# Optimization experiments

Hardware: AMD Instinct MI355X
Metric: run time of the kernel (lower is better)

## Reference

```python
import jax, jax.numpy as jnp
import numpy as np

N_NODES = 20000
N_GRAPH = 256
NODE_DIM = 128
MULS = (128, 64, 32)       # node irreps: 128x0e + 64x1o + 32x2e
HC = 32                    # hidden channels per irrep
HIDDEN_DIM = 64
N_PATH = 9                 # feasible uuw paths into 0e+1e+2e
W_NUMEL = N_PATH * HC * HC # 9216


def _tables():
    # real Clebsch-Gordan tensors built from cartesian tensor algebra,
    # normalized so that sum(C**2) = 2*l_out + 1 (component normalization)
    eps = np.zeros((3, 3, 3))
    eps[0, 1, 2] = eps[1, 2, 0] = eps[2, 0, 1] = 1.0
    eps[0, 2, 1] = eps[2, 1, 0] = eps[1, 0, 2] = -1.0
    s2, s6 = 1 / np.sqrt(2), 1 / np.sqrt(6)
    Q2 = np.zeros((5, 3, 3))  # orthonormal basis of traceless symmetric 3x3
    Q2[0, 0, 1] = Q2[0, 1, 0] = s2          # xy
    Q2[1, 1, 2] = Q2[1, 2, 1] = s2          # yz
    Q2[2, 0, 0] = Q2[2, 1, 1] = -s6; Q2[2, 2, 2] = 2 * s6  # z2
    Q2[3, 0, 2] = Q2[3, 2, 0] = s2          # xz
    Q2[4, 0, 0] = s2; Q2[4, 1, 1] = -s2     # x2-y2

    def nrm(C, l3):
        return C * np.sqrt((2 * l3 + 1) / (C ** 2).sum())

    C000 = np.ones((1, 1, 1))
    C022 = np.eye(5)[None, :, :]
    C110 = np.eye(3).reshape(3, 3, 1) / np.sqrt(3)
    C111 = eps / np.sqrt(2)
    C112 = np.transpose(Q2, (1, 2, 0))
    C202 = np.eye(5)[:, None, :]
    C220 = np.eye(5).reshape(5, 5, 1) / np.sqrt(5)
    M = np.einsum('iab,jdb->ijad', Q2, Q2)  # [5,5,3,3]
    C221 = nrm(np.einsum('cad,ijad->ijc', eps, M), 1)
    S = 0.5 * (M + np.transpose(M, (0, 1, 3, 2)))
    S = S - np.trace(S, axis1=2, axis2=3)[..., None, None] * np.eye(3) / 3.0
    C222 = nrm(np.einsum('kad,ijad->ijk', Q2, S), 2)
    # sph2cart change of basis: 9 spherical comps (0e+1e+2e) -> 3x3 cartesian
    Qc = np.zeros((3, 3, 9))
    Qc[:, :, 0] = np.eye(3) / np.sqrt(3)        # isotropic part
    Qc[:, :, 1:4] = eps / np.sqrt(2)            # antisymmetric part
    Qc[:, :, 4:9] = np.transpose(Q2, (1, 2, 0)) # symmetric traceless part
    return [C000, C022, C110, C111, C112, C202, C220, C221, C222], Qc

_CGS, _QC = _tables()


def setup_inputs() -> dict:
    key = jax.random.key(0)
    ks = jax.random.split(key, 12)
    f32 = jnp.float32
    d_sph = MULS[0] + 3 * MULS[1] + 5 * MULS[2]  # 480
    return {
        'x_scalar': jax.random.normal(ks[0], (N_NODES, NODE_DIM), f32),
        'x_spherical': jax.random.normal(ks[1], (N_NODES, d_sph), f32),
        'batch': jnp.sort(jax.random.randint(ks[2], (N_NODES,), 0, N_GRAPH)),
        'W0e': jax.random.normal(ks[3], (MULS[0], HC), f32),
        'W1o': jax.random.normal(ks[4], (MULS[1], HC), f32),
        'W2e': jax.random.normal(ks[5], (MULS[2], HC), f32),
        'Wm1': jax.random.normal(ks[6], (NODE_DIM, HIDDEN_DIM), f32) / np.sqrt(NODE_DIM),
        'bm1': jnp.zeros((HIDDEN_DIM,), f32),
        'Wm2': jax.random.normal(ks[7], (HIDDEN_DIM, W_NUMEL), f32) / np.sqrt(HIDDEN_DIM),
        'bm2': jnp.zeros((W_NUMEL,), f32),
        'P0': jax.random.normal(ks[8], (3 * HC,), f32),
        'P1': jax.random.normal(ks[9], (2 * HC,), f32),
        'P2': jax.random.normal(ks[10], (4 * HC,), f32),
    }


def reference(x_scalar, x_spherical, batch, W0e, W1o, W2e, Wm1, bm1, Wm2, bm2, P0, P1, P2):
    n = x_scalar.shape[0]
    m0, m1, m2 = MULS
    # split node features into irrep blocks
    x0 = x_spherical[:, :m0, None]                        # [N,128,1] 0e
    x1 = x_spherical[:, m0:m0 + 3 * m1].reshape(n, m1, 3) # [N,64,3]  1o
    x2 = x_spherical[:, m0 + 3 * m1:].reshape(n, m2, 5)   # [N,32,5]  2e
    # pre_lin: per-irrep channel mixing (e3nn-style 1/sqrt(fan_in))
    h = [jnp.einsum('num,uv->nvm', x, W) / np.sqrt(W.shape[0])
         for x, W in ((x0, W0e), (x1, W1o), (x2, W2e))]   # each [N,32,2l+1]
    # per-node tensor-product weights from scalar features
    w = (jax.nn.silu(x_scalar @ Wm1 + bm1) @ Wm2 + bm2).reshape(n, N_PATH, HC, HC)
    # uuw tensor product, path order matches _CGS
    paths = ((0, 0), (0, 2), (1, 1), (1, 1), (1, 1), (2, 0), (2, 2), (2, 2), (2, 2))
    inv_u = 1.0 / np.sqrt(HC)
    outs = []
    for k, (i, j) in enumerate(paths):
        C = jnp.asarray(_CGS[k], x_scalar.dtype)
        outs.append(jnp.einsum('pqr,nup,nuq,nuw->nwr', C, h[i], h[j], w[:, k]) * inv_u)
    # post_lin: combine paths of each output l into a single channel
    y0 = jnp.einsum('num,u->nm', jnp.concatenate([outs[0], outs[2], outs[6]], 1), P0) / np.sqrt(3 * HC)
    y1 = jnp.einsum('num,u->nm', jnp.concatenate([outs[3], outs[7]], 1), P1) / np.sqrt(2 * HC)
    y2 = jnp.einsum('num,u->nm', jnp.concatenate([outs[1], outs[4], outs[5], outs[8]], 1), P2) / np.sqrt(4 * HC)
    sph = jnp.concatenate([y0, y1, y2], axis=1)           # [N,9]
    cart = jnp.einsum('abi,ni->nab', jnp.asarray(_QC, sph.dtype), sph)  # [N,3,3]
    red = jax.ops.segment_sum(cart, batch, num_segments=N_GRAPH)        # [B,3,3]
    # if_trace is False (if_iso=False): roll every non-batch dim by 1
    return jnp.roll(jnp.roll(red, 1, axis=1), 1, axis=2)
```

## Files before the change

kernel.cpp:

```cpp
#include <hip/hip_runtime.h>
#include <math.h>

#define OFF_W2P 0
#define OFF_B2P 12288
#define WS_FLOATS 12480

#define SC_Y0 0.0180421959121758f
#define SC_Y2 0.015625f
#define S2f 0.70710678118654752f
#define S6f 0.40824829046386302f
#define TWOS2f 1.41421356237309505f
#define TWOS6f 0.81649658092772603f
#define ISQRT3 0.57735026918962576f
#define ISQRT5 0.44721359549995794f
#define H0SC 0.08838834764831845f
#define H1SC 0.125f
#define H2SC 0.17677669529663689f

#define COMP(v, q) ((q) == 0 ? (v).x : (q) == 1 ? (v).y : (q) == 2 ? (v).z : (v).w)

__device__ static inline float dot32(const float* __restrict__ a,
                                     const float* __restrict__ b) {
  const float4* a4 = (const float4*)a;
  const float4* b4 = (const float4*)b;
  float acc = 0.f;
#pragma unroll
  for (int q = 0; q < 8; ++q) {
    float4 x = a4[q], y = b4[q];
    acc += x.x * y.x + x.y * y.y + x.z * y.z + x.w * y.w;
  }
  return acc;
}

__global__ __launch_bounds__(256) void prep_kernel(
    const float* __restrict__ Wm2, const float* __restrict__ bm2,
    const float* __restrict__ P0, const float* __restrict__ P2,
    float* __restrict__ ws, float* __restrict__ out) {
  int j = blockIdx.x * 256 + threadIdx.x;
  if (j < 2304) out[j] = 0.f;

  if (j < 12288) {
    const int c = j / 192, o = j % 192;
    const int s = o >> 5, u = o & 31;
    int k; const float* P; float sc;
    switch (s) {
      case 0: k = 0; P = P0;      sc = SC_Y0; break;
      case 1: k = 1; P = P2;      sc = SC_Y2; break;
      case 2: k = 2; P = P0 + 32; sc = SC_Y0; break;
      case 3: k = 4; P = P2 + 32; sc = SC_Y2; break;
      case 4: k = 6; P = P0 + 64; sc = SC_Y0; break;
      default: k = 8; P = P2 + 96; sc = SC_Y2; break;
    }
    float acc = dot32(Wm2 + c * 9216 + k * 1024 + u * 32, P);
    if (s == 1) acc += dot32(Wm2 + c * 9216 + 5 * 1024 + u * 32, P2 + 64);
    ws[OFF_W2P + j] = acc * sc;
  } else if (j < 12480) {
    const int o = j - 12288;
    const int s = o >> 5, u = o & 31;
    int k; const float* P; float sc;
    switch (s) {
      case 0: k = 0; P = P0;      sc = SC_Y0; break;
      case 1: k = 1; P = P2;      sc = SC_Y2; break;
      case 2: k = 2; P = P0 + 32; sc = SC_Y0; break;
      case 3: k = 4; P = P2 + 32; sc = SC_Y2; break;
      case 4: k = 6; P = P0 + 64; sc = SC_Y0; break;
      default: k = 8; P = P2 + 96; sc = SC_Y2; break;
    }
    float acc = dot32(bm2 + k * 1024 + u * 32, P);
    if (s == 1) acc += dot32(bm2 + 5 * 1024 + u * 32, P2 + 64);
    ws[OFF_B2P + o] = acc * sc;
  }
}

__global__ __launch_bounds__(256, 3) void fused_kernel(
    const float* __restrict__ xs_g, const float* __restrict__ xsph,
    const float* __restrict__ W0e, const float* __restrict__ W1o,
    const float* __restrict__ W2e,
    const float* __restrict__ Wm1, const float* __restrict__ bm1,
    const float* __restrict__ ws, const int* __restrict__ batch,
    float* __restrict__ out, const float norm2) {
  __shared__ __align__(16) float smem[11952];
  float (*xp)[484] = (float (*)[484])smem;
  float (*hi2)[64] = (float (*)[64])(smem + 7744);
  float (*Vt)[193] = (float (*)[193])(smem + 8768);
  float (*sphs)[6] = (float (*)[6])(smem + 11856);

  const int tid = threadIdx.x;
  const int n0 = blockIdx.x * 16;

  float4 st[7];
  float4 st7;
#pragma unroll
  for (int k = 0; k < 7; ++k) {
    const int d = tid + k * 256;
    const int r = d / 120, c = d % 120;
    st[k] = *(const float4*)(xsph + (size_t)(n0 + r) * 480 + c * 4);
  }
  if (tid < 128) {
    const int d = tid + 1792;
    const int r = d / 120, c = d % 120;
    st7 = *(const float4*)(xsph + (size_t)(n0 + r) * 480 + c * 4);
  }

  {
    const int n = tid >> 4, c0 = (tid & 15) * 4;
    const float* xr = xs_g + (size_t)(n0 + n) * 128;
    float a0 = 0.f, a1 = 0.f, a2 = 0.f, a3 = 0.f;
#pragma unroll 4
    for (int mq = 0; mq < 32; ++mq) {
      const float4 xv = *(const float4*)(xr + mq * 4);
      const float4 w0 = *(const float4*)(Wm1 + (mq * 4 + 0) * 64 + c0);
      const float4 w1 = *(const float4*)(Wm1 + (mq * 4 + 1) * 64 + c0);
      const float4 w2 = *(const float4*)(Wm1 + (mq * 4 + 2) * 64 + c0);
      const float4 w3 = *(const float4*)(Wm1 + (mq * 4 + 3) * 64 + c0);
      a0 += xv.x * w0.x + xv.y * w1.x + xv.z * w2.x + xv.w * w3.x;
      a1 += xv.x * w0.y + xv.y * w1.y + xv.z * w2.y + xv.w * w3.y;
      a2 += xv.x * w0.z + xv.y * w1.z + xv.z * w2.z + xv.w * w3.z;
      a3 += xv.x * w0.w + xv.y * w1.w + xv.z * w2.w + xv.w * w3.w;
    }
    const float4 bb = *(const float4*)(bm1 + c0);
    const float z0 = a0 + bb.x, z1 = a1 + bb.y, z2 = a2 + bb.z, z3 = a3 + bb.w;
    float4 s;
    s.x = z0 / (1.f + __expf(-z0));
    s.y = z1 / (1.f + __expf(-z1));
    s.z = z2 / (1.f + __expf(-z2));
    s.w = z3 / (1.f + __expf(-z3));
    *(float4*)&hi2[n][c0] = s;
  }

#pragma unroll
  for (int k = 0; k < 7; ++k) {
    const int d = tid + k * 256;
    const int r = d / 120, c = d % 120;
    *(float4*)&xp[r][c * 4] = st[k];
  }
  if (tid < 128) {
    const int d = tid + 1792;
    const int r = d / 120, c = d % 120;
    *(float4*)&xp[r][c * 4] = st7;
  }
  __syncthreads();

  const int n = tid >> 3, ug = tid & 7, u0 = ug * 4;
  float4 acc0 = {0.f, 0.f, 0.f, 0.f};
  float4 acc1[3];
  float4 acc2[5];

  if (tid < 128) {
    const float* row = xp[n];
#pragma unroll 4
    for (int mq = 0; mq < 32; ++mq) {
      const float4 xv = *(const float4*)(row + mq * 4);
#pragma unroll
      for (int r = 0; r < 4; ++r) {
        const float4 w = *(const float4*)(W0e + (mq * 4 + r) * 32 + u0);
        const float xr = COMP(xv, r);
        acc0.x += xr * w.x; acc0.y += xr * w.y;
        acc0.z += xr * w.z; acc0.w += xr * w.w;
      }
    }
#pragma unroll
    for (int j = 0; j < 3; ++j) acc1[j] = make_float4(0.f, 0.f, 0.f, 0.f);
#pragma unroll 2
    for (int mq = 0; mq < 16; ++mq) {
      const float4 b0 = *(const float4*)(row + 128 + mq * 12);
      const float4 b1 = *(const float4*)(row + 128 + mq * 12 + 4);
      const float4 b2 = *(const float4*)(row + 128 + mq * 12 + 8);
      const float xa[12] = {b0.x, b0.y, b0.z, b0.w, b1.x, b1.y, b1.z, b1.w,
                            b2.x, b2.y, b2.z, b2.w};
#pragma unroll
      for (int mm = 0; mm < 4; ++mm) {
        const float4 w = *(const float4*)(W1o + (mq * 4 + mm) * 32 + u0);
#pragma unroll
        for (int j = 0; j < 3; ++j) {
          const float xr = xa[mm * 3 + j];
          acc1[j].x += xr * w.x; acc1[j].y += xr * w.y;
          acc1[j].z += xr * w.z; acc1[j].w += xr * w.w;
        }
      }
    }
#pragma unroll
    for (int j = 0; j < 5; ++j) acc2[j] = make_float4(0.f, 0.f, 0.f, 0.f);
#pragma unroll 2
    for (int mq = 0; mq < 8; ++mq) {
      const float4 c0v = *(const float4*)(row + 320 + mq * 20);
      const float4 c1v = *(const float4*)(row + 320 + mq * 20 + 4);
      const float4 c2v = *(const float4*)(row + 320 + mq * 20 + 8);
      const float4 c3v = *(const float4*)(row + 320 + mq * 20 + 12);
      const float4 c4v = *(const float4*)(row + 320 + mq * 20 + 16);
      const float xa[20] = {c0v.x, c0v.y, c0v.z, c0v.w, c1v.x, c1v.y, c1v.z, c1v.w,
                            c2v.x, c2v.y, c2v.z, c2v.w, c3v.x, c3v.y, c3v.z, c3v.w,
                            c4v.x, c4v.y, c4v.z, c4v.w};
#pragma unroll
      for (int mm = 0; mm < 4; ++mm) {
        const float4 w = *(const float4*)(W2e + (mq * 4 + mm) * 32 + u0);
#pragma unroll
        for (int j = 0; j < 5; ++j) {
          const float xr = xa[mm * 5 + j];
          acc2[j].x += xr * w.x; acc2[j].y += xr * w.y;
          acc2[j].z += xr * w.z; acc2[j].w += xr * w.w;
        }
      }
    }
  } else {
    const int j = tid - 128;
    const bool two = (j < 64);
    const int o2 = j + 128;
    float accA[16], accB[16];
    {
      const float bA = ws[OFF_B2P + j];
#pragma unroll
      for (int nn = 0; nn < 16; ++nn) accA[nn] = bA;
    }
    if (two) {
      const float bB = ws[OFF_B2P + o2];
#pragma unroll
      for (int nn = 0; nn < 16; ++nn) accB[nn] = bB;
    }
    for (int c4 = 0; c4 < 64; c4 += 4) {
      const float wA0 = ws[OFF_W2P + (c4 + 0) * 192 + j];
      const float wA1 = ws[OFF_W2P + (c4 + 1) * 192 + j];
      const float wA2 = ws[OFF_W2P + (c4 + 2) * 192 + j];
      const float wA3 = ws[OFF_W2P + (c4 + 3) * 192 + j];
      float wB0, wB1, wB2, wB3;
      if (two) {
        wB0 = ws[OFF_W2P + (c4 + 0) * 192 + o2];
        wB1 = ws[OFF_W2P + (c4 + 1) * 192 + o2];
        wB2 = ws[OFF_W2P + (c4 + 2) * 192 + o2];
        wB3 = ws[OFF_W2P + (c4 + 3) * 192 + o2];
      }
#pragma unroll
      for (int nn = 0; nn < 16; ++nn) {
        const float4 h = *(const float4*)&hi2[nn][c4];
        accA[nn] += h.x * wA0 + h.y * wA1 + h.z * wA2 + h.w * wA3;
        if (two) accB[nn] += h.x * wB0 + h.y * wB1 + h.z * wB2 + h.w * wB3;
      }
    }
#pragma unroll
    for (int nn = 0; nn < 16; ++nn) {
      Vt[nn][j] = accA[nn];
      if (two) Vt[nn][o2] = accB[nn];
    }
  }
  __syncthreads();

  if (tid < 128) {
    float y0s = 0.f;
    float y2s[5] = {0.f, 0.f, 0.f, 0.f, 0.f};
#pragma unroll
    for (int q = 0; q < 4; ++q) {
      const int u = u0 + q;
      const float* Vp = &Vt[n][u];
      const float v0 = Vp[0], v15 = Vp[32], v2 = Vp[64], v3 = Vp[96];
      const float v5 = Vp[128], v6 = Vp[160];

      const float h0 = COMP(acc0, q) * H0SC;
      const float h1a = COMP(acc1[0], q) * H1SC;
      const float h1b = COMP(acc1[1], q) * H1SC;
      const float h1c = COMP(acc1[2], q) * H1SC;
      float h2v[5];
#pragma unroll
      for (int jj = 0; jj < 5; ++jj) h2v[jj] = COMP(acc2[jj], q) * H2SC;

      const float d11 = h1a * h1a + h1b * h1b + h1c * h1c;
      const float d22 = h2v[0] * h2v[0] + h2v[1] * h2v[1] + h2v[2] * h2v[2] +
                        h2v[3] * h2v[3] + h2v[4] * h2v[4];
      float y0 = v0 * h0 * h0 + v2 * d11 * ISQRT3 + v5 * d22 * ISQRT5;

      const float o00 = h1a * h1a, o01 = h1a * h1b, o02 = h1a * h1c;
      const float o11 = h1b * h1b, o12 = h1b * h1c, o22 = h1c * h1c;
      const float t40 = TWOS2f * o01, t41 = TWOS2f * o12;
      const float t42 = S6f * (2.f * o22 - o00 - o11);
      const float t43 = TWOS2f * o02, t44 = S2f * (o00 - o11);

      const float A00 = -S6f * h2v[2] + S2f * h2v[4];
      const float A01 = S2f * h2v[0];
      const float A02 = S2f * h2v[3];
      const float A11 = -S6f * h2v[2] - S2f * h2v[4];
      const float A12 = S2f * h2v[1];
      const float A22 = TWOS6f * h2v[2];
      const float B00 = A00 * A00 + A01 * A01 + A02 * A02;
      const float B01 = A00 * A01 + A01 * A11 + A02 * A12;
      const float B02 = A00 * A02 + A01 * A12 + A02 * A22;
      const float B11 = A01 * A01 + A11 * A11 + A12 * A12;
      const float B12 = A01 * A02 + A11 * A12 + A12 * A22;
      const float B22 = A02 * A02 + A12 * A12 + A22 * A22;
      const float t80 = TWOS2f * B01, t81 = TWOS2f * B12;
      const float t82 = S6f * (2.f * B22 - B00 - B11);
      const float t83 = TWOS2f * B02, t84 = S2f * (B00 - B11);

      const float w15 = v15 * h0;
      const float v6n = v6 * norm2;
      y0s += y0;
      y2s[0] += w15 * h2v[0] + v3 * t40 + v6n * t80;
      y2s[1] += w15 * h2v[1] + v3 * t41 + v6n * t81;
      y2s[2] += w15 * h2v[2] + v3 * t42 + v6n * t82;
      y2s[3] += w15 * h2v[3] + v3 * t43 + v6n * t83;
      y2s[4] += w15 * h2v[4] + v3 * t44 + v6n * t84;
    }

#pragma unroll
    for (int off = 4; off > 0; off >>= 1) {
      y0s += __shfl_xor(y0s, off, 8);
#pragma unroll
      for (int r = 0; r < 5; ++r) y2s[r] += __shfl_xor(y2s[r], off, 8);
    }

    if (ug == 0) {
      sphs[n][0] = y0s;
#pragma unroll
      for (int r = 0; r < 5; ++r) sphs[n][1 + r] = y2s[r];
    }
  }
  __syncthreads();

  if (tid < 9) {
    const float QW[9][6] = {
        {ISQRT3, 0.f, 0.f, -S6f, 0.f, S2f},
        {0.f, S2f, 0.f, 0.f, 0.f, 0.f},
        {0.f, 0.f, 0.f, 0.f, S2f, 0.f},
        {0.f, S2f, 0.f, 0.f, 0.f, 0.f},
        {ISQRT3, 0.f, 0.f, -S6f, 0.f, -S2f},
        {0.f, 0.f, S2f, 0.f, 0.f, 0.f},
        {0.f, 0.f, 0.f, 0.f, S2f, 0.f},
        {0.f, 0.f, S2f, 0.f, 0.f, 0.f},
        {ISQRT3, 0.f, 0.f, TWOS6f, 0.f, 0.f}};
    const int a = tid / 3, b = tid % 3;
    const int rolled = ((a + 1) % 3) * 3 + ((b + 1) % 3);
    const float c0 = QW[tid][0], c1 = QW[tid][1], c2 = QW[tid][2];
    const float c3 = QW[tid][3], c4 = QW[tid][4], c5 = QW[tid][5];
    int cur_g = batch[n0];
    float acc = 0.f;
#pragma unroll
    for (int q = 0; q < 16; ++q) {
      const int g = batch[n0 + q];
      const float val = c0 * sphs[q][0] + c1 * sphs[q][1] + c2 * sphs[q][2] +
                        c3 * sphs[q][3] + c4 * sphs[q][4] + c5 * sphs[q][5];
      if (g != cur_g) {
        atomicAdd(out + cur_g * 9 + rolled, acc);
        acc = 0.f;
        cur_g = g;
      }
      acc += val;
    }
    atomicAdd(out + cur_g * 9 + rolled, acc);
  }
}

extern "C" void kernel_launch(void* const* d_in, const int* in_sizes, int n_in,
                              void* d_out, int out_size, void* d_ws, size_t ws_size,
                              hipStream_t stream) {
  const float* x_scalar = (const float*)d_in[0];
  const float* x_sph    = (const float*)d_in[1];
  const int*   batch    = (const int*)d_in[2];
  const float* W0e      = (const float*)d_in[3];
  const float* W1o      = (const float*)d_in[4];
  const float* W2e      = (const float*)d_in[5];
  const float* Wm1      = (const float*)d_in[6];
  const float* bm1      = (const float*)d_in[7];
  const float* Wm2      = (const float*)d_in[8];
  const float* bm2      = (const float*)d_in[9];
  const float* P0       = (const float*)d_in[10];
  const float* P2       = (const float*)d_in[12];
  float* ws  = (float*)d_ws;
  float* out = (float*)d_out;

  if (ws_size < (size_t)WS_FLOATS * sizeof(float)) return;

  double Q2[5][3][3] = {};
  const double s2d = 0.70710678118654752440, s6d = 0.40824829046386301637;
  Q2[0][0][1] = Q2[0][1][0] = s2d;
  Q2[1][1][2] = Q2[1][2][1] = s2d;
  Q2[2][0][0] = Q2[2][1][1] = -s6d; Q2[2][2][2] = 2.0 * s6d;
  Q2[3][0][2] = Q2[3][2][0] = s2d;
  Q2[4][0][0] = s2d; Q2[4][1][1] = -s2d;
  double ss = 0.0;
  for (int i = 0; i < 5; ++i)
    for (int jj = 0; jj < 5; ++jj) {
      double S[3][3];
      for (int a = 0; a < 3; ++a)
        for (int d = 0; d < 3; ++d) {
          double m1 = 0, m2 = 0;
          for (int b = 0; b < 3; ++b) {
            m1 += Q2[i][a][b] * Q2[jj][d][b];
            m2 += Q2[i][d][b] * Q2[jj][a][b];
          }
          S[a][d] = 0.5 * (m1 + m2);
        }
      double tr = (S[0][0] + S[1][1] + S[2][2]) / 3.0;
      S[0][0] -= tr; S[1][1] -= tr; S[2][2] -= tr;
      for (int kk = 0; kk < 5; ++kk) {
        double cc = 0;
        for (int a = 0; a < 3; ++a)
          for (int d = 0; d < 3; ++d) cc += Q2[kk][a][d] * S[a][d];
        ss += cc * cc;
      }
    }
  const float norm2 = (float)sqrt(5.0 / ss);

  prep_kernel<<<49, 256, 0, stream>>>(Wm2, bm2, P0, P2, ws, out);
  fused_kernel<<<1250, 256, 0, stream>>>(x_scalar, x_sph, W0e, W1o, W2e,
                                         Wm1, bm1, ws, batch, out, norm2);
}
```

Measured before the change: 158.8 us.

## Process 32 nodes per block and serialize projection and weight-GEMM phases

Each block now handles 32 nodes instead of 16, with all 256 threads doing the per-node linear projections. A separate phase follows in which 192 threads compute the hidden-to-weight GEMM for all 32 nodes. That GEMM's output buffer aliases the staged input in shared memory, so a barrier separates the two phases. This removes the earlier split where half the threads did projections while the other half did the GEMM, and halves the grid to amortize per-block weight loads. In exchange it adds a barrier and raises shared memory and register pressure (32 accumulators per thread, 15 staged float4s), while the launch bound now asks for 4 blocks per CU.

```diff
diff --git a/kernel.cpp b/kernel.cpp
--- a/kernel.cpp
+++ b/kernel.cpp
@@ -72,179 +72,162 @@
   }
 }
 
-__global__ __launch_bounds__(256, 3) void fused_kernel(
+__global__ __launch_bounds__(256, 4) void fused_kernel(
     const float* __restrict__ xs_g, const float* __restrict__ xsph,
     const float* __restrict__ W0e, const float* __restrict__ W1o,
     const float* __restrict__ W2e,
     const float* __restrict__ Wm1, const float* __restrict__ bm1,
     const float* __restrict__ ws, const int* __restrict__ batch,
     float* __restrict__ out, const float norm2) {
-  __shared__ __align__(16) float smem[11952];
+  __shared__ __align__(16) float smem[17728];
   float (*xp)[484] = (float (*)[484])smem;
-  float (*hi2)[64] = (float (*)[64])(smem + 7744);
-  float (*Vt)[193] = (float (*)[193])(smem + 8768);
-  float (*sphs)[6] = (float (*)[6])(smem + 11856);
+  float (*Vt)[193] = (float (*)[193])smem;
+  float (*hi2)[64] = (float (*)[64])(smem + 15488);
+  float (*sphs)[6] = (float (*)[6])(smem + 17536);
 
   const int tid = threadIdx.x;
-  const int n0 = blockIdx.x * 16;
-
-  float4 st[7];
-  float4 st7;
-#pragma unroll
-  for (int k = 0; k < 7; ++k) {
+  const int n0 = blockIdx.x * 32;
+
+  float4 st[15];
+#pragma unroll
+  for (int k = 0; k < 15; ++k) {
     const int d = tid + k * 256;
     const int r = d / 120, c = d % 120;
     st[k] = *(const float4*)(xsph + (size_t)(n0 + r) * 480 + c * 4);
   }
-  if (tid < 128) {
-    const int d = tid + 1792;
-    const int r = d / 120, c = d % 120;
-    st7 = *(const float4*)(xsph + (size_t)(n0 + r) * 480 + c * 4);
-  }
 
   {
-    const int n = tid >> 4, c0 = (tid & 15) * 4;
-    const float* xr = xs_g + (size_t)(n0 + n) * 128;
-    float a0 = 0.f, a1 = 0.f, a2 = 0.f, a3 = 0.f;
+    const int nb = (tid >> 4) * 2, c0 = (tid & 15) * 4;
+    const float* xrA = xs_g + (size_t)(n0 + nb) * 128;
+    const float* xrB = xrA + 128;
+    float accA[4] = {0.f, 0.f, 0.f, 0.f};
+    float accB[4] = {0.f, 0.f, 0.f, 0.f};
 #pragma unroll 4
     for (int mq = 0; mq < 32; ++mq) {
-      const float4 xv = *(const float4*)(xr + mq * 4);
-      const float4 w0 = *(const float4*)(Wm1 + (mq * 4 + 0) * 64 + c0);
-      const float4 w1 = *(const float4*)(Wm1 + (mq * 4 + 1) * 64 + c0);
-      const float4 w2 = *(const float4*)(Wm1 + (mq * 4 + 2) * 64 + c0);
-      const float4 w3 = *(const float4*)(Wm1 + (mq * 4 + 3) * 64 + c0);
-      a0 += xv.x * w0.x + xv.y * w1.x + xv.z * w2.x + xv.w * w3.x;
-      a1 += xv.x * w0.y + xv.y * w1.y + xv.z * w2.y + xv.w * w3.y;
-      a2 += xv.x * w0.z + xv.y * w1.z + xv.z * w2.z + xv.w * w3.z;
-      a3 += xv.x * w0.w + xv.y * w1.w + xv.z * w2.w + xv.w * w3.w;
+      const float4 xa = *(const float4*)(xrA + mq * 4);
+      const float4 xb = *(const float4*)(xrB + mq * 4);
+#pragma unroll
+      for (int r = 0; r < 4; ++r) {
+        const float4 w = *(const float4*)(Wm1 + (mq * 4 + r) * 64 + c0);
+        const float fa = COMP(xa, r), fb = COMP(xb, r);
+        accA[0] += fa * w.x; accA[1] += fa * w.y; accA[2] += fa * w.z; accA[3] += fa * w.w;
+        accB[0] += fb * w.x; accB[1] += fb * w.y; accB[2] += fb * w.z; accB[3] += fb * w.w;
+      }
     }
     const float4 bb = *(const float4*)(bm1 + c0);
-    const float z0 = a0 + bb.x, z1 = a1 + bb.y, z2 = a2 + bb.z, z3 = a3 + bb.w;
-    float4 s;
-    s.x = z0 / (1.f + __expf(-z0));
-    s.y = z1 / (1.f + __expf(-z1));
-    s.z = z2 / (1.f + __expf(-z2));
-    s.w = z3 / (1.f + __expf(-z3));
-    *(float4*)&hi2[n][c0] = s;
-  }
-
-#pragma unroll
-  for (int k = 0; k < 7; ++k) {
+    const float ba[4] = {bb.x, bb.y, bb.z, bb.w};
+    float4 sA, sB;
+    {
+      const float z0 = accA[0] + ba[0], z1 = accA[1] + ba[1];
+      const float z2 = accA[2] + ba[2], z3 = accA[3] + ba[3];
+      sA.x = z0 / (1.f + __expf(-z0)); sA.y = z1 / (1.f + __expf(-z1));
+      sA.z = z2 / (1.f + __expf(-z2)); sA.w = z3 / (1.f + __expf(-z3));
+    }
+    {
+      const float z0 = accB[0] + ba[0], z1 = accB[1] + ba[1];
+      const float z2 = accB[2] + ba[2], z3 = accB[3] + ba[3];
+      sB.x = z0 / (1.f + __expf(-z0)); sB.y = z1 / (1.f + __expf(-z1));
+      sB.z = z2 / (1.f + __expf(-z2)); sB.w = z3 / (1.f + __expf(-z3));
+    }
+    *(float4*)&hi2[nb][c0] = sA;
+    *(float4*)&hi2[nb + 1][c0] = sB;
+  }
+
+#pragma unroll
+  for (int k = 0; k < 15; ++k) {
     const int d = tid + k * 256;
     const int r = d / 120, c = d % 120;
     *(float4*)&xp[r][c * 4] = st[k];
   }
-  if (tid < 128) {
-    const int d = tid + 1792;
-    const int r = d / 120, c = d % 120;
-    *(float4*)&xp[r][c * 4] = st7;
-  }
   __syncthreads();
 
   const int n = tid >> 3, ug = tid & 7, u0 = ug * 4;
+  const float* row = xp[n];
   float4 acc0 = {0.f, 0.f, 0.f, 0.f};
   float4 acc1[3];
   float4 acc2[5];
 
-  if (tid < 128) {
-    const float* row = xp[n];
 #pragma unroll 4
-    for (int mq = 0; mq < 32; ++mq) {
-      const float4 xv = *(const float4*)(row + mq * 4);
-#pragma unroll
-      for (int r = 0; r < 4; ++r) {
-        const float4 w = *(const float4*)(W0e + (mq * 4 + r) * 32 + u0);
-        const float xr = COMP(xv, r);
-        acc0.x += xr * w.x; acc0.y += xr * w.y;
-        acc0.z += xr * w.z; acc0.w += xr * w.w;
-      }
-    }
-#pragma unroll
-    for (int j = 0; j < 3; ++j) acc1[j] = make_float4(0.f, 0.f, 0.f, 0.f);
+  for (int mq = 0; mq < 32; ++mq) {
+    const float4 xv = *(const float4*)(row + mq * 4);
+#pragma unroll
+    for (int r = 0; r < 4; ++r) {
+      const float4 w = *(const float4*)(W0e + (mq * 4 + r) * 32 + u0);
+      const float xr = COMP(xv, r);
+      acc0.x += xr * w.x; acc0.y += xr * w.y;
+      acc0.z += xr * w.z; acc0.w += xr * w.w;
+    }
+  }
+#pragma unroll
+  for (int j = 0; j < 3; ++j) acc1[j] = make_float4(0.f, 0.f, 0.f, 0.f);
 #pragma unroll 2
-    for (int mq = 0; mq < 16; ++mq) {
-      const float4 b0 = *(const float4*)(row + 128 + mq * 12);
-      const float4 b1 = *(const float4*)(row + 128 + mq * 12 + 4);
-      const float4 b2 = *(const float4*)(row + 128 + mq * 12 + 8);
-      const float xa[12] = {b0.x, b0.y, b0.z, b0.w, b1.x, b1.y, b1.z, b1.w,
-                            b2.x, b2.y, b2.z, b2.w};
-#pragma unroll
-      for (int mm = 0; mm < 4; ++mm) {
-        const float4 w = *(const float4*)(W1o + (mq * 4 + mm) * 32 + u0);
-#pragma unroll
-        for (int j = 0; j < 3; ++j) {
-          const float xr = xa[mm * 3 + j];
-          acc1[j].x += xr * w.x; acc1[j].y += xr * w.y;
-          acc1[j].z += xr * w.z; acc1[j].w += xr * w.w;
-        }
-      }
-    }
-#pragma unroll
-    for (int j = 0; j < 5; ++j) acc2[j] = make_float4(0.f, 0.f, 0.f, 0.f);
+  for (int mq = 0; mq < 16; ++mq) {
+    const float4 b0 = *(const float4*)(row + 128 + mq * 12);
+    const float4 b1 = *(const float4*)(row + 128 + mq * 12 + 4);
+    const float4 b2 = *(const float4*)(row + 128 + mq * 12 + 8);
+    const float xa[12] = {b0.x, b0.y, b0.z, b0.w, b1.x, b1.y, b1.z, b1.w,
+                          b2.x, b2.y, b2.z, b2.w};
+#pragma unroll
+    for (int mm = 0; mm < 4; ++mm) {
+      const float4 w = *(const float4*)(W1o + (mq * 4 + mm) * 32 + u0);
+#pragma unroll
+      for (int j = 0; j < 3; ++j) {
+        const float xr = xa[mm * 3 + j];
+        acc1[j].x += xr * w.x; acc1[j].y += xr * w.y;
+        acc1[j].z += xr * w.z; acc1[j].w += xr * w.w;
+      }
+    }
+  }
+#pragma unroll
+  for (int j = 0; j < 5; ++j) acc2[j] = make_float4(0.f, 0.f, 0.f, 0.f);
 #pragma unroll 2
-    for (int mq = 0; mq < 8; ++mq) {
-      const float4 c0v = *(const float4*)(row + 320 + mq * 20);
-      const float4 c1v = *(const float4*)(row + 320 + mq * 20 + 4);
-      const float4 c2v = *(const float4*)(row + 320 + mq * 20 + 8);
-      const float4 c3v = *(const float4*)(row + 320 + mq * 20 + 12);
-      const float4 c4v = *(const float4*)(row + 320 + mq * 20 + 16);
-      const float xa[20] = {c0v.x, c0v.y, c0v.z, c0v.w, c1v.x, c1v.y, c1v.z, c1v.w,
-                            c2v.x, c2v.y, c2v.z, c2v.w, c3v.x, c3v.y, c3v.z, c3v.w,
-                            c4v.x, c4v.y, c4v.z, c4v.w};
-#pragma unroll
-      for (int mm = 0; mm < 4; ++mm) {
-        const float4 w = *(const float4*)(W2e + (mq * 4 + mm) * 32 + u0);
-#pragma unroll
-        for (int j = 0; j < 5; ++j) {
-          const float xr = xa[mm * 5 + j];
-          acc2[j].x += xr * w.x; acc2[j].y += xr * w.y;
-          acc2[j].z += xr * w.z; acc2[j].w += xr * w.w;
-        }
-      }
-    }
-  } else {
-    const int j = tid - 128;
-    const bool two = (j < 64);
-    const int o2 = j + 128;
-    float accA[16], accB[16];
+  for (int mq = 0; mq < 8; ++mq) {
+    const float4 c0v = *(const float4*)(row + 320 + mq * 20);
+    const float4 c1v = *(const float4*)(row + 320 + mq * 20 + 4);
+    const float4 c2v = *(const float4*)(row + 320 + mq * 20 + 8);
+    const float4 c3v = *(const float4*)(row + 320 + mq * 20 + 12);
+    const float4 c4v = *(const float4*)(row + 320 + mq * 20 + 16);
+    const float xa[20] = {c0v.x, c0v.y, c0v.z, c0v.w, c1v.x, c1v.y, c1v.z, c1v.w,
+                          c2v.x, c2v.y, c2v.z, c2v.w, c3v.x, c3v.y, c3v.z, c3v.w,
+                          c4v.x, c4v.y, c4v.z, c4v.w};
+#pragma unroll
+    for (int mm = 0; mm < 4; ++mm) {
+      const float4 w = *(const float4*)(W2e + (mq * 4 + mm) * 32 + u0);
+#pragma unroll
+      for (int j = 0; j < 5; ++j) {
+        const float xr = xa[mm * 5 + j];
+        acc2[j].x += xr * w.x; acc2[j].y += xr * w.y;
+        acc2[j].z += xr * w.z; acc2[j].w += xr * w.w;
+      }
+    }
+  }
+  __syncthreads();
+
+  if (tid < 192) {
+    const int o = tid;
+    float acc[32];
     {
-      const float bA = ws[OFF_B2P + j];
-#pragma unroll
-      for (int nn = 0; nn < 16; ++nn) accA[nn] = bA;
-    }
-    if (two) {
-      const float bB = ws[OFF_B2P + o2];
-#pragma unroll
-      for (int nn = 0; nn < 16; ++nn) accB[nn] = bB;
+      const float b = ws[OFF_B2P + o];
+#pragma unroll
+      for (int nn = 0; nn < 32; ++nn) acc[nn] = b;
     }
     for (int c4 = 0; c4 < 64; c4 += 4) {
-      const float wA0 = ws[OFF_W2P + (c4 + 0) * 192 + j];
-      const float wA1 = ws[OFF_W2P + (c4 + 1) * 192 + j];
-      const float wA2 = ws[OFF_W2P + (c4 + 2) * 192 + j];
-      const float wA3 = ws[OFF_W2P + (c4 + 3) * 192 + j];
-      float wB0, wB1, wB2, wB3;
-      if (two) {
-        wB0 = ws[OFF_W2P + (c4 + 0) * 192 + o2];
-        wB1 = ws[OFF_W2P + (c4 + 1) * 192 + o2];
-        wB2 = ws[OFF_W2P + (c4 + 2) * 192 + o2];
-        wB3 = ws[OFF_W2P + (c4 + 3) * 192 + o2];
-      }
-#pragma unroll
-      for (int nn = 0; nn < 16; ++nn) {
+      const float w0 = ws[OFF_W2P + (c4 + 0) * 192 + o];
+      const float w1 = ws[OFF_W2P + (c4 + 1) * 192 + o];
+      const float w2 = ws[OFF_W2P + (c4 + 2) * 192 + o];
+      const float w3 = ws[OFF_W2P + (c4 + 3) * 192 + o];
+#pragma unroll
+      for (int nn = 0; nn < 32; ++nn) {
         const float4 h = *(const float4*)&hi2[nn][c4];
-        accA[nn] += h.x * wA0 + h.y * wA1 + h.z * wA2 + h.w * wA3;
-        if (two) accB[nn] += h.x * wB0 + h.y * wB1 + h.z * wB2 + h.w * wB3;
-      }
-    }
-#pragma unroll
-    for (int nn = 0; nn < 16; ++nn) {
-      Vt[nn][j] = accA[nn];
-      if (two) Vt[nn][o2] = accB[nn];
-    }
+        acc[nn] += h.x * w0 + h.y * w1 + h.z * w2 + h.w * w3;
+      }
+    }
+#pragma unroll
+    for (int nn = 0; nn < 32; ++nn) Vt[nn][o] = acc[nn];
   }
   __syncthreads();
 
-  if (tid < 128) {
+  {
     float y0s = 0.f;
     float y2s[5] = {0.f, 0.f, 0.f, 0.f, 0.f};
 #pragma unroll
@@ -265,7 +248,7 @@
       const float d11 = h1a * h1a + h1b * h1b + h1c * h1c;
       const float d22 = h2v[0] * h2v[0] + h2v[1] * h2v[1] + h2v[2] * h2v[2] +
                         h2v[3] * h2v[3] + h2v[4] * h2v[4];
-      float y0 = v0 * h0 * h0 + v2 * d11 * ISQRT3 + v5 * d22 * ISQRT5;
+      const float y0 = v0 * h0 * h0 + v2 * d11 * ISQRT3 + v5 * d22 * ISQRT5;
 
       const float o00 = h1a * h1a, o01 = h1a * h1b, o02 = h1a * h1c;
       const float o11 = h1b * h1b, o12 = h1b * h1c, o22 = h1c * h1c;
@@ -332,7 +315,7 @@
     int cur_g = batch[n0];
     float acc = 0.f;
 #pragma unroll
-    for (int q = 0; q < 16; ++q) {
+    for (int q = 0; q < 32; ++q) {
       const int g = batch[n0 + q];
       const float val = c0 * sphs[q][0] + c1 * sphs[q][1] + c2 * sphs[q][2] +
                         c3 * sphs[q][3] + c4 * sphs[q][4] + c5 * sphs[q][5];
@@ -399,6 +382,6 @@
   const float norm2 = (float)sqrt(5.0 / ss);
 
   prep_kernel<<<49, 256, 0, stream>>>(Wm2, bm2, P0, P2, ws, out);
-  fused_kernel<<<1250, 256, 0, stream>>>(x_scalar, x_sph, W0e, W1o, W2e,
-                                         Wm1, bm1, ws, batch, out, norm2);
+  fused_kernel<<<625, 256, 0, stream>>>(x_scalar, x_sph, W0e, W1o, W2e,
+                                        Wm1, bm1, ws, batch, out, norm2);
 }
```

New measurement: 174.7 us. +10.0%, slower.

## Alias Vt onto xp buffer and split phases across all 256 threads

Applied to the files above, without the earlier changes.

The kernel used to split its threads: half did the irrep projections and half did the hidden-to-path matmul at the same time. Now all 256 threads do the projections first, with 2 channels per thread instead of 4, and a barrier follows. Then 192 threads do the matmul, writing Vt into shared memory that aliases the now-dead xp buffer. This cuts shared memory per block and raises the launch-bounds occupancy target from 3 to 4 blocks. The cost is one extra barrier and serialising two phases that previously ran concurrently.

```diff
diff --git a/kernel.cpp b/kernel.cpp
--- a/kernel.cpp
+++ b/kernel.cpp
@@ -72,18 +72,18 @@
   }
 }
 
-__global__ __launch_bounds__(256, 3) void fused_kernel(
+__global__ __launch_bounds__(256, 4) void fused_kernel(
     const float* __restrict__ xs_g, const float* __restrict__ xsph,
     const float* __restrict__ W0e, const float* __restrict__ W1o,
     const float* __restrict__ W2e,
     const float* __restrict__ Wm1, const float* __restrict__ bm1,
     const float* __restrict__ ws, const int* __restrict__ batch,
     float* __restrict__ out, const float norm2) {
-  __shared__ __align__(16) float smem[11952];
+  __shared__ __align__(16) float smem[8864];
   float (*xp)[484] = (float (*)[484])smem;
+  float (*Vt)[193] = (float (*)[193])smem;
   float (*hi2)[64] = (float (*)[64])(smem + 7744);
-  float (*Vt)[193] = (float (*)[193])(smem + 8768);
-  float (*sphs)[6] = (float (*)[6])(smem + 11856);
+  float (*sphs)[6] = (float (*)[6])(smem + 8768);
 
   const int tid = threadIdx.x;
   const int n0 = blockIdx.x * 16;
@@ -141,131 +141,112 @@
   }
   __syncthreads();
 
-  const int n = tid >> 3, ug = tid & 7, u0 = ug * 4;
-  float4 acc0 = {0.f, 0.f, 0.f, 0.f};
-  float4 acc1[3];
-  float4 acc2[5];
-
-  if (tid < 128) {
-    const float* row = xp[n];
+  const int n = tid >> 4, ug = tid & 15, u0 = ug * 2;
+  const float* row = xp[n];
+  float2 acc0 = {0.f, 0.f};
+  float2 acc1[3];
+  float2 acc2[5];
+
 #pragma unroll 4
-    for (int mq = 0; mq < 32; ++mq) {
-      const float4 xv = *(const float4*)(row + mq * 4);
-#pragma unroll
-      for (int r = 0; r < 4; ++r) {
-        const float4 w = *(const float4*)(W0e + (mq * 4 + r) * 32 + u0);
-        const float xr = COMP(xv, r);
-        acc0.x += xr * w.x; acc0.y += xr * w.y;
-        acc0.z += xr * w.z; acc0.w += xr * w.w;
-      }
-    }
-#pragma unroll
-    for (int j = 0; j < 3; ++j) acc1[j] = make_float4(0.f, 0.f, 0.f, 0.f);
+  for (int mq = 0; mq < 32; ++mq) {
+    const float4 xv = *(const float4*)(row + mq * 4);
+#pragma unroll
+    for (int r = 0; r < 4; ++r) {
+      const float2 w = *(const float2*)(W0e + (mq * 4 + r) * 32 + u0);
+      const float xr = COMP(xv, r);
+      acc0.x += xr * w.x; acc0.y += xr * w.y;
+    }
+  }
+#pragma unroll
+  for (int j = 0; j < 3; ++j) acc1[j] = make_float2(0.f, 0.f);
 #pragma unroll 2
-    for (int mq = 0; mq < 16; ++mq) {
-      const float4 b0 = *(const float4*)(row + 128 + mq * 12);
-      const float4 b1 = *(const float4*)(row + 128 + mq * 12 + 4);
-      const float4 b2 = *(const float4*)(row + 128 + mq * 12 + 8);
-      const float xa[12] = {b0.x, b0.y, b0.z, b0.w, b1.x, b1.y, b1.z, b1.w,
-                            b2.x, b2.y, b2.z, b2.w};
-#pragma unroll
-      for (int mm = 0; mm < 4; ++mm) {
-        const float4 w = *(const float4*)(W1o + (mq * 4 + mm) * 32 + u0);
-#pragma unroll
-        for (int j = 0; j < 3; ++j) {
-          const float xr = xa[mm * 3 + j];
-          acc1[j].x += xr * w.x; acc1[j].y += xr * w.y;
-          acc1[j].z += xr * w.z; acc1[j].w += xr * w.w;
-        }
-      }
-    }
-#pragma unroll
-    for (int j = 0; j < 5; ++j) acc2[j] = make_float4(0.f, 0.f, 0.f, 0.f);
+  for (int mq = 0; mq < 16; ++mq) {
+    const float4 b0 = *(const float4*)(row + 128 + mq * 12);
+    const float4 b1 = *(const float4*)(row + 128 + mq * 12 + 4);
+    const float4 b2 = *(const float4*)(row + 128 + mq * 12 + 8);
+    const float xa[12] = {b0.x, b0.y, b0.z, b0.w, b1.x, b1.y, b1.z, b1.w,
+                          b2.x, b2.y, b2.z, b2.w};
+#pragma unroll
+    for (int mm = 0; mm < 4; ++mm) {
+      const float2 w = *(const float2*)(W1o + (mq * 4 + mm) * 32 + u0);
+#pragma unroll
+      for (int j = 0; j < 3; ++j) {
+        const float xr = xa[mm * 3 + j];
+        acc1[j].x += xr * w.x; acc1[j].y += xr * w.y;
+      }
+    }
+  }
+#pragma unroll
+  for (int j = 0; j < 5; ++j) acc2[j] = make_float2(0.f, 0.f);
 #pragma unroll 2
-    for (int mq = 0; mq < 8; ++mq) {
-      const float4 c0v = *(const float4*)(row + 320 + mq * 20);
-      const float4 c1v = *(const float4*)(row + 320 + mq * 20 + 4);
-      const float4 c2v = *(const float4*)(row + 320 + mq * 20 + 8);
-      const float4 c3v = *(const float4*)(row + 320 + mq * 20 + 12);
-      const float4 c4v = *(const float4*)(row + 320 + mq * 20 + 16);
-      const float xa[20] = {c0v.x, c0v.y, c0v.z, c0v.w, c1v.x, c1v.y, c1v.z, c1v.w,
-                            c2v.x, c2v.y, c2v.z, c2v.w, c3v.x, c3v.y, c3v.z, c3v.w,
-                            c4v.x, c4v.y, c4v.z, c4v.w};
-#pragma unroll
-      for (int mm = 0; mm < 4; ++mm) {
-        const float4 w = *(const float4*)(W2e + (mq * 4 + mm) * 32 + u0);
-#pragma unroll
-        for (int j = 0; j < 5; ++j) {
-          const float xr = xa[mm * 5 + j];
-          acc2[j].x += xr * w.x; acc2[j].y += xr * w.y;
-          acc2[j].z += xr * w.z; acc2[j].w += xr * w.w;
-        }
-      }
-    }
-  } else {
-    const int j = tid - 128;
-    const bool two = (j < 64);
-    const int o2 = j + 128;
-    float accA[16], accB[16];
+  for (int mq = 0; mq < 8; ++mq) {
+    const float4 c0v = *(const float4*)(row + 320 + mq * 20);
+    const float4 c1v = *(const float4*)(row + 320 + mq * 20 + 4);
+    const float4 c2v = *(const float4*)(row + 320 + mq * 20 + 8);
+    const float4 c3v = *(const float4*)(row + 320 + mq * 20 + 12);
+    const float4 c4v = *(const float4*)(row + 320 + mq * 20 + 16);
+    const float xa[20] = {c0v.x, c0v.y, c0v.z, c0v.w, c1v.x, c1v.y, c1v.z, c1v.w,
+                          c2v.x, c2v.y, c2v.z, c2v.w, c3v.x, c3v.y, c3v.z, c3v.w,
+                          c4v.x, c4v.y, c4v.z, c4v.w};
+#pragma unroll
+    for (int mm = 0; mm < 4; ++mm) {
+      const float2 w = *(const float2*)(W2e + (mq * 4 + mm) * 32 + u0);
+#pragma unroll
+      for (int j = 0; j < 5; ++j) {
+        const float xr = xa[mm * 5 + j];
+        acc2[j].x += xr * w.x; acc2[j].y += xr * w.y;
+      }
+    }
+  }
+  __syncthreads();
+
+  if (tid < 192) {
+    const int o = tid;
+    float acc[16];
     {
-      const float bA = ws[OFF_B2P + j];
-#pragma unroll
-      for (int nn = 0; nn < 16; ++nn) accA[nn] = bA;
-    }
-    if (two) {
-      const float bB = ws[OFF_B2P + o2];
-#pragma unroll
-      for (int nn = 0; nn < 16; ++nn) accB[nn] = bB;
+      const float b = ws[OFF_B2P + o];
+#pragma unroll
+      for (int nn = 0; nn < 16; ++nn) acc[nn] = b;
     }
     for (int c4 = 0; c4 < 64; c4 += 4) {
-      const float wA0 = ws[OFF_W2P + (c4 + 0) * 192 + j];
-      const float wA1 = ws[OFF_W2P + (c4 + 1) * 192 + j];
-      const float wA2 = ws[OFF_W2P + (c4 + 2) * 192 + j];
-      const float wA3 = ws[OFF_W2P + (c4 + 3) * 192 + j];
-      float wB0, wB1, wB2, wB3;
-      if (two) {
-        wB0 = ws[OFF_W2P + (c4 + 0) * 192 + o2];
-        wB1 = ws[OFF_W2P + (c4 + 1) * 192 + o2];
-        wB2 = ws[OFF_W2P + (c4 + 2) * 192 + o2];
-        wB3 = ws[OFF_W2P + (c4 + 3) * 192 + o2];
-      }
+      const float w0 = ws[OFF_W2P + (c4 + 0) * 192 + o];
+      const float w1 = ws[OFF_W2P + (c4 + 1) * 192 + o];
+      const float w2 = ws[OFF_W2P + (c4 + 2) * 192 + o];
+      const float w3 = ws[OFF_W2P + (c4 + 3) * 192 + o];
 #pragma unroll
       for (int nn = 0; nn < 16; ++nn) {
         const float4 h = *(const float4*)&hi2[nn][c4];
-        accA[nn] += h.x * wA0 + h.y * wA1 + h.z * wA2 + h.w * wA3;
-        if (two) accB[nn] += h.x * wB0 + h.y * wB1 + h.z * wB2 + h.w * wB3;
-      }
-    }
-#pragma unroll
-    for (int nn = 0; nn < 16; ++nn) {
-      Vt[nn][j] = accA[nn];
-      if (two) Vt[nn][o2] = accB[nn];
-    }
+        acc[nn] += h.x * w0 + h.y * w1 + h.z * w2 + h.w * w3;
+      }
+    }
+#pragma unroll
+    for (int nn = 0; nn < 16; ++nn) Vt[nn][o] = acc[nn];
   }
   __syncthreads();
 
-  if (tid < 128) {
+  {
     float y0s = 0.f;
     float y2s[5] = {0.f, 0.f, 0.f, 0.f, 0.f};
 #pragma unroll
-    for (int q = 0; q < 4; ++q) {
+    for (int q = 0; q < 2; ++q) {
       const int u = u0 + q;
       const float* Vp = &Vt[n][u];
       const float v0 = Vp[0], v15 = Vp[32], v2 = Vp[64], v3 = Vp[96];
       const float v5 = Vp[128], v6 = Vp[160];
 
-      const float h0 = COMP(acc0, q) * H0SC;
-      const float h1a = COMP(acc1[0], q) * H1SC;
-      const float h1b = COMP(acc1[1], q) * H1SC;
-      const float h1c = COMP(acc1[2], q) * H1SC;
+      const float h0 = (q == 0 ? acc0.x : acc0.y) * H0SC;
+      const float h1a = (q == 0 ? acc1[0].x : acc1[0].y) * H1SC;
+      const float h1b = (q == 0 ? acc1[1].x : acc1[1].y) * H1SC;
+      const float h1c = (q == 0 ? acc1[2].x : acc1[2].y) * H1SC;
       float h2v[5];
 #pragma unroll
-      for (int jj = 0; jj < 5; ++jj) h2v[jj] = COMP(acc2[jj], q) * H2SC;
+      for (int jj = 0; jj < 5; ++jj)
+        h2v[jj] = (q == 0 ? acc2[jj].x : acc2[jj].y) * H2SC;
 
       const float d11 = h1a * h1a + h1b * h1b + h1c * h1c;
       const float d22 = h2v[0] * h2v[0] + h2v[1] * h2v[1] + h2v[2] * h2v[2] +
                         h2v[3] * h2v[3] + h2v[4] * h2v[4];
-      float y0 = v0 * h0 * h0 + v2 * d11 * ISQRT3 + v5 * d22 * ISQRT5;
+      const float y0 = v0 * h0 * h0 + v2 * d11 * ISQRT3 + v5 * d22 * ISQRT5;
 
       const float o00 = h1a * h1a, o01 = h1a * h1b, o02 = h1a * h1c;
       const float o11 = h1b * h1b, o12 = h1b * h1c, o22 = h1c * h1c;
@@ -300,10 +281,10 @@
     }
 
 #pragma unroll
-    for (int off = 4; off > 0; off >>= 1) {
-      y0s += __shfl_xor(y0s, off, 8);
-#pragma unroll
-      for (int r = 0; r < 5; ++r) y2s[r] += __shfl_xor(y2s[r], off, 8);
+    for (int off = 8; off > 0; off >>= 1) {
+      y0s += __shfl_xor(y0s, off, 16);
+#pragma unroll
+      for (int r = 0; r < 5; ++r) y2s[r] += __shfl_xor(y2s[r], off, 16);
     }
 
     if (ug == 0) {
```

Result: slower. 166.6 us (+4.9%).
